# Performance work log

Hardware: AMD Instinct MI355X
Metric: run time of the kernel (lower is better)

## Reference

```python
import jax, jax.numpy as jnp
import numpy as np

BS, UE, RX, D = 4, 8, 128, 64
D_OUT = 64


def setup_inputs() -> dict:
    key = jax.random.key(0)
    ks = jax.random.split(key, 8)
    s1 = 1.0 / np.sqrt(5 * D)
    s2 = 1.0 / np.sqrt(D)
    return {
        "x": jax.random.normal(ks[0], (BS, UE, RX, D), dtype=jnp.float32),
        "W1": jax.random.uniform(ks[1], (D, 5 * D), jnp.float32, -s1, s1),
        "b1": jax.random.uniform(ks[2], (D,), jnp.float32, -s1, s1),
        "ln_g": jnp.ones((D,), jnp.float32),
        "ln_b": jnp.zeros((D,), jnp.float32),
        "bias": jnp.zeros((D,), jnp.float32),
        "W2": jax.random.uniform(ks[3], (D_OUT, D), jnp.float32, -s2, s2),
        "b2": jax.random.uniform(ks[4], (D_OUT,), jnp.float32, -s2, s2),
    }


def reference(x, W1, b1, ln_g, ln_b, bias, W2, b2):
    bs, ue, rx, d = x.shape
    # diagonal mask [rx, rx, 1] broadcast over feature dim
    diag = jnp.eye(rx, dtype=x.dtype)[:, :, None]
    m = jnp.mean(x, axis=2, keepdims=True)          # [bs, ue, 1, d]
    # Five pairwise feature maps, each [bs, ue, rx, rx, d]
    x1 = x[:, :, :, None, :] * diag                 # diag_embed(x)
    x2 = jnp.broadcast_to(x[:, :, :, None, :], (bs, ue, rx, rx, d))  # row copy
    x3 = jnp.broadcast_to(x[:, :, None, :, :], (bs, ue, rx, rx, d))  # col copy
    x4 = m[:, :, :, None, :] * diag                 # diag_embed(mean)
    x5 = jnp.broadcast_to(m[:, :, :, None, :], (bs, ue, rx, rx, d))  # mean bcast
    xAll = jnp.concatenate([x1, x2, x3, x4, x5], axis=-1)  # [bs, ue, rx, rx, 5d]
    # fc1
    h = jnp.einsum("buijf,df->buijd", xAll, W1) + b1
    # LayerNorm over last dim (eps = 1e-5, torch default)
    mu = jnp.mean(h, axis=-1, keepdims=True)
    var = jnp.mean(jnp.square(h - mu), axis=-1, keepdims=True)
    h = (h - mu) * jax.lax.rsqrt(var + 1e-5) * ln_g + ln_b
    y = jax.nn.relu(h)
    # diagonal-masked learned bias
    y = y + bias * diag
    # fc2
    out = jnp.einsum("buijd,od->buijo", y, W2) + b2
    return out
```

## Files before the change

### kernel.cpp

```cpp
#include <hip/hip_runtime.h>
#include <stdint.h>

#define RX 128
#define ROWS 4096
#define NBU 32

typedef __attribute__((ext_vector_type(8))) short short8;
typedef __attribute__((ext_vector_type(4))) float f32x4;

#define WS_R1 0
#define WS_R2 262144
#define WS_R3 524288
#define WS_R4 786432
#define WS_R5 788480

__device__ __forceinline__ short bf16rne(float f) {
    uint32_t u = __float_as_uint(f);
    u += 0x7FFFu + ((u >> 16) & 1u);
    return (short)(u >> 16);
}

__device__ __forceinline__ void ld16f(const float* __restrict__ p, int d0, int d1,
                                      float* __restrict__ o) {
    *(float4*)(o + 0)  = *(const float4*)(p + d0);
    *(float4*)(o + 4)  = *(const float4*)(p + d0 + 4);
    *(float4*)(o + 8)  = *(const float4*)(p + d1);
    *(float4*)(o + 12) = *(const float4*)(p + d1 + 4);
}

__global__ __launch_bounds__(192) void k_pre(const float* __restrict__ x,
                                             const float* __restrict__ W1,
                                             const float* __restrict__ b1,
                                             float* __restrict__ ws) {
    __shared__ float s[8256];
    const int t = threadIdx.x;
    const int blk = blockIdx.x;

    if (blk < 512) {
        const int r0 = blk * 8;
        if (t < 128)
            ((float4*)s)[t] = ((const float4*)(x + r0 * 64))[t];
        __syncthreads();
        const int arr = t >> 6;
        const int dp  = t & 63;
        const float* wrow = W1 + dp * 320 + arr * 64;
        float4 w[16];
#pragma unroll
        for (int fc = 0; fc < 16; ++fc) w[fc] = ((const float4*)wrow)[fc];
        float* dst = ws + (arr == 0 ? WS_R1 : arr == 1 ? WS_R2 : WS_R3);
#pragma unroll
        for (int r = 0; r < 8; ++r) {
            float acc = 0.f;
#pragma unroll
            for (int fc = 0; fc < 16; ++fc) {
                float4 xv = ((const float4*)(s + r * 64))[fc];
                acc = fmaf(xv.x, w[fc].x, acc);
                acc = fmaf(xv.y, w[fc].y, acc);
                acc = fmaf(xv.z, w[fc].z, acc);
                acc = fmaf(xv.w, w[fc].w, acc);
            }
            dst[(r0 + r) * 64 + dp] = acc;
        }
    } else {
        const int bu = blk - 512;
        const float* xb = x + bu * RX * 64;
        for (int idx = t; idx < 2048; idx += 192)
            ((float4*)s)[idx] = ((const float4*)xb)[idx];
        __syncthreads();
        if (t < 64) {
            float a0 = 0, a1 = 0, a2 = 0, a3 = 0;
            for (int r = 0; r < 128; r += 4) {
                a0 += s[(r + 0) * 64 + t];
                a1 += s[(r + 1) * 64 + t];
                a2 += s[(r + 2) * 64 + t];
                a3 += s[(r + 3) * 64 + t];
            }
            s[8192 + t] = (a0 + a1 + a2 + a3) * (1.0f / 128.0f);
        }
        __syncthreads();
        if (t < 128) {
            const int dp = t & 63, which = t >> 6;
            const float* wrow = W1 + dp * 320 + 192 + which * 64;
            float acc = which ? b1[dp] : 0.f;
#pragma unroll
            for (int fc = 0; fc < 16; ++fc) {
                float4 mv = ((const float4*)(s + 8192))[fc];
                float4 wv = ((const float4*)wrow)[fc];
                acc = fmaf(mv.x, wv.x, acc);
                acc = fmaf(mv.y, wv.y, acc);
                acc = fmaf(mv.z, wv.z, acc);
                acc = fmaf(mv.w, wv.w, acc);
            }
            (ws + (which ? WS_R5 : WS_R4))[bu * 64 + dp] = acc;
        }
    }
}

__global__ __launch_bounds__(256) void k_main(const float* __restrict__ ws,
                                              const float* __restrict__ ln_g,
                                              const float* __restrict__ ln_b,
                                              const float* __restrict__ bias,
                                              const float* __restrict__ W2,
                                              const float* __restrict__ b2,
                                              float* __restrict__ out) {
    const float* R1  = ws + WS_R1;
    const float* R2  = ws + WS_R2;
    const float* R3  = ws + WS_R3;
    const float* r4  = ws + WS_R4;
    const float* r5b = ws + WS_R5;

    const int t    = threadIdx.x;
    const int lane = t & 63;
    const int wid  = t >> 6;
    const int q    = lane >> 4;
    const int ml   = lane & 15;
    const int row  = blockIdx.x;
    const int bu   = row >> 7;
    const int i    = row & 127;

    const int d0 = q * 8;
    const int d1 = 32 + q * 8;

    float basev[16], tmp[16], gv[16], bbv[16];
    ld16f(R2 + row * 64, d0, d1, basev);
    ld16f(r5b + bu * 64, d0, d1, tmp);
#pragma unroll
    for (int s = 0; s < 16; ++s) basev[s] += tmp[s];
    ld16f(ln_g, d0, d1, gv);
    ld16f(ln_b, d0, d1, bbv);

    short8 bf[4][2];
#pragma unroll
    for (int ot = 0; ot < 4; ++ot) {
#pragma unroll
        for (int kt = 0; kt < 2; ++kt) {
            const float* wp = W2 + (ot * 16 + ml) * 64 + kt * 32 + q * 8;
            float4 w0 = *(const float4*)wp;
            float4 w1 = *(const float4*)(wp + 4);
            short8 v;
            v[0] = bf16rne(w0.x); v[1] = bf16rne(w0.y);
            v[2] = bf16rne(w0.z); v[3] = bf16rne(w0.w);
            v[4] = bf16rne(w1.x); v[5] = bf16rne(w1.y);
            v[6] = bf16rne(w1.z); v[7] = bf16rne(w1.w);
            bf[ot][kt] = v;
        }
    }
    float b2v[4];
#pragma unroll
    for (int ot = 0; ot < 4; ++ot) b2v[ot] = b2[ot * 16 + ml];

    const float* r3base = R3 + (size_t)bu * 128 * 64;
    float* outB = out + (size_t)row * 8192;
    const int it = i >> 4, im = i & 15;

#pragma unroll
    for (int p = 0; p < 2; ++p) {
        const int jt = p * 4 + wid;
        const int j  = jt * 16 + ml;

        float h[16];
        ld16f(r3base + j * 64, d0, d1, h);
#pragma unroll
        for (int s = 0; s < 16; ++s) h[s] += basev[s];

        const bool diag = (jt == it) && (ml == im);
        if (jt == it) {
            if (diag) {
                float da[16], db[16];
                ld16f(R1 + row * 64, d0, d1, da);
                ld16f(r4 + bu * 64, d0, d1, db);
#pragma unroll
                for (int s = 0; s < 16; ++s) h[s] += da[s] + db[s];
            }
        }

        float sum = 0.f, ss = 0.f;
#pragma unroll
        for (int s = 0; s < 16; ++s) { sum += h[s]; ss = fmaf(h[s], h[s], ss); }
        sum += __shfl_xor(sum, 16); sum += __shfl_xor(sum, 32);
        ss  += __shfl_xor(ss, 16);  ss  += __shfl_xor(ss, 32);
        const float mu  = sum * 0.015625f;
        const float var = ss * 0.015625f - mu * mu;
        const float inv = rsqrtf(var + 1e-5f);

        float y[16];
#pragma unroll
        for (int s = 0; s < 16; ++s) {
            float v = fmaf((h[s] - mu) * inv, gv[s], bbv[s]);
            y[s] = fmaxf(v, 0.f);
        }
        if (diag) {
            float bi[16];
            ld16f(bias, d0, d1, bi);
#pragma unroll
            for (int s = 0; s < 16; ++s) y[s] += bi[s];
        }

        short8 a0, a1;
#pragma unroll
        for (int jj = 0; jj < 8; ++jj) { a0[jj] = bf16rne(y[jj]); a1[jj] = bf16rne(y[8 + jj]); }

#pragma unroll
        for (int ot = 0; ot < 4; ++ot) {
            f32x4 acc = { b2v[ot], b2v[ot], b2v[ot], b2v[ot] };
            acc = __builtin_amdgcn_mfma_f32_16x16x32_bf16(a0, bf[ot][0], acc, 0, 0, 0);
            acc = __builtin_amdgcn_mfma_f32_16x16x32_bf16(a1, bf[ot][1], acc, 0, 0, 0);
            float* ob = outB + (size_t)(jt * 16 + q * 4) * 64 + ot * 16 + ml;
            ob[0]   = acc[0];
            ob[64]  = acc[1];
            ob[128] = acc[2];
            ob[192] = acc[3];
        }
    }
}

extern "C" void kernel_launch(void* const* d_in, const int* in_sizes, int n_in,
                              void* d_out, int out_size, void* d_ws, size_t ws_size,
                              hipStream_t stream) {
    const float* x    = (const float*)d_in[0];
    const float* W1   = (const float*)d_in[1];
    const float* b1   = (const float*)d_in[2];
    const float* ln_g = (const float*)d_in[3];
    const float* ln_b = (const float*)d_in[4];
    const float* bias = (const float*)d_in[5];
    const float* W2   = (const float*)d_in[6];
    const float* b2   = (const float*)d_in[7];
    float* ws  = (float*)d_ws;
    float* out = (float*)d_out;

    hipLaunchKernelGGL(k_pre, dim3(544), dim3(192), 0, stream, x, W1, b1, ws);
    hipLaunchKernelGGL(k_main, dim3(4096), dim3(256), 0, stream,
                       ws, ln_g, ln_b, bias, W2, b2, out);
}
```

Before: 197.9 us.

## Stage R3 slice in LDS and process two rows per block

The R3 column block for each (batch, ue) pair is now loaded once into padded shared memory, and each block handles two i-rows instead of one. This halves the grid and replaces repeated global loads of R3 with LDS reads. In exchange each block pays a 34KB LDS tile plus a barrier and does twice the work. The kernel is dominated by the 128MB output write, so the gain may be limited.

After: 175.0 us. 1.13x faster.

```diff
diff --git a/kernel.cpp b/kernel.cpp
--- a/kernel.cpp
+++ b/kernel.cpp
@@ -13,6 +13,8 @@
 #define WS_R3 524288
 #define WS_R4 786432
 #define WS_R5 788480
+
+#define LDP 68
 
 __device__ __forceinline__ short bf16rne(float f) {
     uint32_t u = __float_as_uint(f);
@@ -109,23 +111,31 @@
     const float* r4  = ws + WS_R4;
     const float* r5b = ws + WS_R5;
 
+    __shared__ float sR3[128 * LDP];
+
     const int t    = threadIdx.x;
     const int lane = t & 63;
     const int wid  = t >> 6;
     const int q    = lane >> 4;
     const int ml   = lane & 15;
-    const int row  = blockIdx.x;
-    const int bu   = row >> 7;
-    const int i    = row & 127;
+    const int bu   = blockIdx.x >> 6;
+    const int i0   = (blockIdx.x & 63) * 2;
 
     const int d0 = q * 8;
     const int d1 = 32 + q * 8;
 
-    float basev[16], tmp[16], gv[16], bbv[16];
-    ld16f(R2 + row * 64, d0, d1, basev);
-    ld16f(r5b + bu * 64, d0, d1, tmp);
-#pragma unroll
-    for (int s = 0; s < 16; ++s) basev[s] += tmp[s];
+    {
+        const float* r3g = R3 + (size_t)bu * 8192;
+#pragma unroll
+        for (int c = 0; c < 8; ++c) {
+            const int g = c * 256 + t;
+            const int r = g >> 4, col = (g & 15) << 2;
+            *(float4*)&sR3[r * LDP + col] = ((const float4*)r3g)[g];
+        }
+    }
+
+    float r5v[16], gv[16], bbv[16];
+    ld16f(r5b + bu * 64, d0, d1, r5v);
     ld16f(ln_g, d0, d1, gv);
     ld16f(ln_b, d0, d1, bbv);
 
@@ -149,67 +159,83 @@
 #pragma unroll
     for (int ot = 0; ot < 4; ++ot) b2v[ot] = b2[ot * 16 + ml];
 
-    const float* r3base = R3 + (size_t)bu * 128 * 64;
-    float* outB = out + (size_t)row * 8192;
-    const int it = i >> 4, im = i & 15;
-
-#pragma unroll
-    for (int p = 0; p < 2; ++p) {
-        const int jt = p * 4 + wid;
-        const int j  = jt * 16 + ml;
-
-        float h[16];
-        ld16f(r3base + j * 64, d0, d1, h);
-#pragma unroll
-        for (int s = 0; s < 16; ++s) h[s] += basev[s];
-
-        const bool diag = (jt == it) && (ml == im);
-        if (jt == it) {
+    __syncthreads();
+
+#pragma unroll
+    for (int ip = 0; ip < 2; ++ip) {
+        const int i   = i0 + ip;
+        const int row = bu * 128 + i;
+        const int it  = i >> 4, im = i & 15;
+
+        float basev[16], tmp[16];
+        ld16f(R2 + (size_t)row * 64, d0, d1, basev);
+#pragma unroll
+        for (int s = 0; s < 16; ++s) basev[s] += r5v[s];
+
+        float* outB = out + (size_t)row * 8192;
+
+#pragma unroll
+        for (int p = 0; p < 2; ++p) {
+            const int jt = p * 4 + wid;
+            const int j  = jt * 16 + ml;
+
+            float h[16];
+            {
+                const float* sp = sR3 + j * LDP;
+                *(float4*)(h + 0)  = *(const float4*)(sp + d0);
+                *(float4*)(h + 4)  = *(const float4*)(sp + d0 + 4);
+                *(float4*)(h + 8)  = *(const float4*)(sp + d1);
+                *(float4*)(h + 12) = *(const float4*)(sp + d1 + 4);
+            }
+#pragma unroll
+            for (int s = 0; s < 16; ++s) h[s] += basev[s];
+
+            const bool diag = (jt == it) && (ml == im);
             if (diag) {
                 float da[16], db[16];
-                ld16f(R1 + row * 64, d0, d1, da);
+                ld16f(R1 + (size_t)row * 64, d0, d1, da);
                 ld16f(r4 + bu * 64, d0, d1, db);
 #pragma unroll
                 for (int s = 0; s < 16; ++s) h[s] += da[s] + db[s];
             }
-        }
-
-        float sum = 0.f, ss = 0.f;
-#pragma unroll
-        for (int s = 0; s < 16; ++s) { sum += h[s]; ss = fmaf(h[s], h[s], ss); }
-        sum += __shfl_xor(sum, 16); sum += __shfl_xor(sum, 32);
-        ss  += __shfl_xor(ss, 16);  ss  += __shfl_xor(ss, 32);
-        const float mu  = sum * 0.015625f;
-        const float var = ss * 0.015625f - mu * mu;
-        const float inv = rsqrtf(var + 1e-5f);
-
-        float y[16];
-#pragma unroll
-        for (int s = 0; s < 16; ++s) {
-            float v = fmaf((h[s] - mu) * inv, gv[s], bbv[s]);
-            y[s] = fmaxf(v, 0.f);
-        }
-        if (diag) {
-            float bi[16];
-            ld16f(bias, d0, d1, bi);
-#pragma unroll
-            for (int s = 0; s < 16; ++s) y[s] += bi[s];
-        }
-
-        short8 a0, a1;
-#pragma unroll
-        for (int jj = 0; jj < 8; ++jj) { a0[jj] = bf16rne(y[jj]); a1[jj] = bf16rne(y[8 + jj]); }
-
-#pragma unroll
-        for (int ot = 0; ot < 4; ++ot) {
-            f32x4 acc = { b2v[ot], b2v[ot], b2v[ot], b2v[ot] };
-            acc = __builtin_amdgcn_mfma_f32_16x16x32_bf16(a0, bf[ot][0], acc, 0, 0, 0);
-            acc = __builtin_amdgcn_mfma_f32_16x16x32_bf16(a1, bf[ot][1], acc, 0, 0, 0);
-            float* ob = outB + (size_t)(jt * 16 + q * 4) * 64 + ot * 16 + ml;
-            ob[0]   = acc[0];
-            ob[64]  = acc[1];
-            ob[128] = acc[2];
-            ob[192] = acc[3];
+
+            float sum = 0.f, ss = 0.f;
+#pragma unroll
+            for (int s = 0; s < 16; ++s) { sum += h[s]; ss = fmaf(h[s], h[s], ss); }
+            sum += __shfl_xor(sum, 16); sum += __shfl_xor(sum, 32);
+            ss  += __shfl_xor(ss, 16);  ss  += __shfl_xor(ss, 32);
+            const float mu  = sum * 0.015625f;
+            const float var = ss * 0.015625f - mu * mu;
+            const float inv = rsqrtf(var + 1e-5f);
+
+            float y[16];
+#pragma unroll
+            for (int s = 0; s < 16; ++s) {
+                float v = fmaf((h[s] - mu) * inv, gv[s], bbv[s]);
+                y[s] = fmaxf(v, 0.f);
+            }
+            if (diag) {
+                float bi[16];
+                ld16f(bias, d0, d1, bi);
+#pragma unroll
+                for (int s = 0; s < 16; ++s) y[s] += bi[s];
+            }
+
+            short8 a0, a1;
+#pragma unroll
+            for (int jj = 0; jj < 8; ++jj) { a0[jj] = bf16rne(y[jj]); a1[jj] = bf16rne(y[8 + jj]); }
+
+#pragma unroll
+            for (int ot = 0; ot < 4; ++ot) {
+                f32x4 acc = { b2v[ot], b2v[ot], b2v[ot], b2v[ot] };
+                acc = __builtin_amdgcn_mfma_f32_16x16x32_bf16(a0, bf[ot][0], acc, 0, 0, 0);
+                acc = __builtin_amdgcn_mfma_f32_16x16x32_bf16(a1, bf[ot][1], acc, 0, 0, 0);
+                float* ob = outB + (size_t)(jt * 16 + q * 4) * 64 + ot * 16 + ml;
+                ob[0]   = acc[0];
+                ob[64]  = acc[1];
+                ob[128] = acc[2];
+                ob[192] = acc[3];
+            }
         }
     }
 }
@@ -229,6 +255,6 @@
     float* out = (float*)d_out;
 
     hipLaunchKernelGGL(k_pre, dim3(544), dim3(192), 0, stream, x, W1, b1, ws);
-    hipLaunchKernelGGL(k_main, dim3(4096), dim3(256), 0, stream,
+    hipLaunchKernelGGL(k_main, dim3(2048), dim3(256), 0, stream,
                        ws, ln_g, ln_b, bias, W2, b2, out);
 }
```
